# Kernel tuning notes

Measured on AMD Instinct MI355X. Metric: run time of the kernel, lower is better.

## Reference

```python
import jax, jax.numpy as jnp
import numpy as np

EMBED = 1024
HEADS = 16
HEAD_DIM = EMBED // HEADS
FFN = 4096
B, S = 2, 2048
EPS = 1e-5


def setup_inputs() -> dict:
    key = jax.random.key(0)
    ks = jax.random.split(key, 16)
    sc = 0.02
    return {
        "x": jax.random.normal(ks[0], (B, S, EMBED), jnp.float32),
        "rope_cos": jax.random.uniform(ks[1], (S, HEAD_DIM), jnp.float32),
        "rope_sin": jax.random.uniform(ks[2], (S, HEAD_DIM), jnp.float32),
        "Wq": jax.random.normal(ks[3], (EMBED, EMBED), jnp.float32) * sc,
        "bq": jnp.zeros((EMBED,), jnp.float32),
        "Wk": jax.random.normal(ks[4], (EMBED, EMBED), jnp.float32) * sc,
        "bk": jnp.zeros((EMBED,), jnp.float32),
        "Wv": jax.random.normal(ks[5], (EMBED, EMBED), jnp.float32) * sc,
        "bv": jnp.zeros((EMBED,), jnp.float32),
        "Wo": jax.random.normal(ks[6], (EMBED, EMBED), jnp.float32) * sc,
        "bo": jnp.zeros((EMBED,), jnp.float32),
        "W1": jax.random.normal(ks[7], (EMBED, FFN), jnp.float32) * sc,
        "b1": jnp.zeros((FFN,), jnp.float32),
        "W2": jax.random.normal(ks[8], (FFN, EMBED), jnp.float32) * sc,
        "b2": jnp.zeros((EMBED,), jnp.float32),
        "g1": jnp.ones((EMBED,), jnp.float32),
        "be1": jnp.zeros((EMBED,), jnp.float32),
        "g2": jnp.ones((EMBED,), jnp.float32),
        "be2": jnp.zeros((EMBED,), jnp.float32),
    }


def _layernorm(x, g, b):
    mu = jnp.mean(x, axis=-1, keepdims=True)
    var = jnp.var(x, axis=-1, keepdims=True)
    return (x - mu) * jax.lax.rsqrt(var + EPS) * g + b


def _rotate_half(x):
    half = x.shape[-1] // 2
    return jnp.concatenate((-x[..., half:], x[..., :half]), axis=-1)


def _apply_rope(x, cos, sin):
    # x: (B, H, S, D); cos/sin: (S, D)
    return x * cos[None, None] + _rotate_half(x) * sin[None, None]


def reference(x, rope_cos, rope_sin, Wq, bq, Wk, bk, Wv, bv, Wo, bo,
              W1, b1, W2, b2, g1, be1, g2, be2):
    batch, seq_len, embed = x.shape
    n = _layernorm(x, g1, be1)

    def heads(t):
        return t.reshape(batch, seq_len, HEADS, HEAD_DIM).transpose(0, 2, 1, 3)

    q = heads(n @ Wq + bq)
    k = heads(n @ Wk + bk)
    v = heads(n @ Wv + bv)
    q = _apply_rope(q, rope_cos, rope_sin)
    k = _apply_rope(k, rope_cos, rope_sin)

    scale = 1.0 / np.sqrt(HEAD_DIM)
    scores = jnp.einsum("bhqd,bhkd->bhqk", q, k) * scale  # (B,H,S,S)
    causal = jnp.triu(jnp.ones((seq_len, seq_len), bool), k=1)
    scores = jnp.where(causal[None, None], -jnp.inf, scores)
    attn = jax.nn.softmax(scores, axis=-1)
    out = jnp.einsum("bhqk,bhkd->bhqd", attn, v)
    out = out.transpose(0, 2, 1, 3).reshape(batch, seq_len, embed)
    x = x + (out @ Wo + bo)

    n2 = _layernorm(x, g2, be2)
    h = jax.nn.gelu(n2 @ W1 + b1, approximate=False)
    x = x + (h @ W2 + b2)
    return x
```

## Files before the change

kernel.cpp:

```cpp
#include <hip/hip_runtime.h>
#include <math.h>

#define EMBED 1024
#define SLEN  2048
#define BATCH 2
#define HEADS 16
#define HD    64
#define FFN_D 4096
#define MROWS (BATCH*SLEN)

typedef short bh8  __attribute__((ext_vector_type(8)));
typedef float f32x4 __attribute__((ext_vector_type(4)));
typedef __attribute__((address_space(3))) const short* lsp;

#define MFMA16(a,b,c) __builtin_amdgcn_mfma_f32_16x16x32_bf16((a),(b),(c),0,0,0)
#define GLDS16(g,l) __builtin_amdgcn_global_load_lds( \
    (__attribute__((address_space(1))) void*)(g), \
    (__attribute__((address_space(3))) void*)(l), 16, 0, 0)
#define DSR(dst, base, IMM) \
  asm volatile("ds_read_b128 %0, %1 offset:" #IMM : "=v"(dst) : "v"(base))

__device__ inline float b2f(short s) {
  union { unsigned u; float f; } c; c.u = ((unsigned)(unsigned short)s) << 16; return c.f;
}
__device__ inline short f2b(float f) {
  union { float f; unsigned u; } c; c.f = f;
  unsigned r = (c.u + 0x7FFFu + ((c.u >> 16) & 1u)) >> 16;
  return (short)r;
}
__device__ inline float exp2a(float x) {
  float r; asm("v_exp_f32 %0, %1" : "=v"(r) : "v"(x)); return r;
}

__global__ __launch_bounds__(256) void transpose_w(const float* __restrict__ in,
                                                   short* __restrict__ out,
                                                   int K, int N) {
  __shared__ short sm[64][65];
  const int tid = threadIdx.x;
  const int k0 = blockIdx.y * 64, n0 = blockIdx.x * 64;
#pragma unroll
  for (int it = 0; it < 16; ++it) {
    int idx = it * 256 + tid;
    int r = idx >> 6, c = idx & 63;
    sm[r][c] = f2b(in[(size_t)(k0 + r) * N + n0 + c]);
  }
  __syncthreads();
#pragma unroll
  for (int it = 0; it < 16; ++it) {
    int idx = it * 256 + tid;
    int r = idx >> 6, c = idx & 63;
    out[(size_t)(n0 + r) * K + k0 + c] = sm[c][r];
  }
}

__global__ __launch_bounds__(256) void transpose_v(const short* __restrict__ in,
                                                   short* __restrict__ out) {
  __shared__ short sm[64][65];
  const int tid = threadIdx.x;
  const int s0 = blockIdx.x * 64, bh = blockIdx.y;
  const int b = bh >> 4, h = bh & 15;
#pragma unroll
  for (int it = 0; it < 16; ++it) {
    int idx = it * 256 + tid;
    int r = idx >> 6, c = idx & 63;
    sm[r][c] = in[((size_t)(b*SLEN + s0 + r))*EMBED + h*HD + c];
  }
  __syncthreads();
#pragma unroll
  for (int it = 0; it < 16; ++it) {
    int idx = it * 256 + tid;
    int r = idx >> 6, c = idx & 63;
    out[((size_t)(bh*HD + r))*SLEN + s0 + c] = sm[c][r];
  }
}

__global__ __launch_bounds__(256) void ln_kernel(const float* __restrict__ inF,
                                                 const short* __restrict__ inB,
                                                 const float* __restrict__ gw,
                                                 const float* __restrict__ bw,
                                                 short* __restrict__ out) {
  const int row = blockIdx.x, tid = threadIdx.x;
  const int w = tid >> 6;
  const size_t base = (size_t)row * EMBED;
  float x[4];
#pragma unroll
  for (int i = 0; i < 4; ++i) {
    int c = tid + i * 256;
    x[i] = inF ? inF[base + c] : b2f(inB[base + c]);
  }
  float s = x[0] + x[1] + x[2] + x[3];
  float ss = x[0]*x[0] + x[1]*x[1] + x[2]*x[2] + x[3]*x[3];
#pragma unroll
  for (int off = 32; off >= 1; off >>= 1) { s += __shfl_xor(s, off); ss += __shfl_xor(ss, off); }
  __shared__ float red[8];
  if ((tid & 63) == 0) { red[w*2] = s; red[w*2+1] = ss; }
  __syncthreads();
  s  = red[0] + red[2] + red[4] + red[6];
  ss = red[1] + red[3] + red[5] + red[7];
  const float mu = s * (1.0f/EMBED);
  const float var = ss * (1.0f/EMBED) - mu*mu;
  const float rstd = rsqrtf(var + 1e-5f);
#pragma unroll
  for (int i = 0; i < 4; ++i) {
    int c = tid + i * 256;
    out[base + c] = f2b((x[i]-mu)*rstd*gw[c] + bw[c]);
  }
}

__global__ __launch_bounds__(256, 2) void gemm_bt(const short* __restrict__ A,
                                                  const short* __restrict__ Bt,
                                                  const float* __restrict__ bias0,
                                                  const float* __restrict__ bias1,
                                                  const float* __restrict__ bias2,
                                                  float* __restrict__ outF,
                                                  short* __restrict__ outB0,
                                                  short* __restrict__ outB1,
                                                  short* __restrict__ outB2,
                                                  const float* __restrict__ residF,
                                                  const short* __restrict__ residB,
                                                  const float* __restrict__ ropeCos,
                                                  const float* __restrict__ ropeSin,
                                                  int N, int K, int gelu, int qkv) {
  __shared__ short As[16384];
  __shared__ short Bs[16384];
  const int tid = threadIdx.x;
  const int w = tid >> 6, L = tid & 63;
  const int quad = L >> 4, l16 = L & 15;

  int bx = blockIdx.x, by = blockIdx.y;
  {
    const int gx = gridDim.x;
    const int nwg = gx * gridDim.y;
    const int wg = by*gx + bx;
    const int swz = (wg & 7)*(nwg >> 3) + (wg >> 3);
    bx = swz % gx; by = swz / gx;
  }
  const int bm = by * 128, bn = bx * 128;
  const int wm = (w >> 1) * 64, wn = (w & 1) * 64;
  const int NT = K >> 6;

  f32x4 acc[4][4];
#pragma unroll
  for (int i = 0; i < 4; ++i)
#pragma unroll
    for (int j = 0; j < 4; ++j) acc[i][j] = (f32x4){0.f,0.f,0.f,0.f};

  const int c0i = tid, c1i = 256 + tid;
  const int r0i = c0i >> 2, s0i = (c0i & 3) ^ ((r0i >> 1) & 3);
  const int r1i = c1i >> 2, s1i = (c1i & 3) ^ ((r1i >> 1) & 3);
  const short* aG0 = A  + (size_t)(bm + r0i)*K + s0i*8;
  const short* aG1 = A  + (size_t)(bm + r1i)*K + s1i*8;
  const short* bG0 = Bt + (size_t)(bn + r0i)*K + s0i*8;
  const short* bG1 = Bt + (size_t)(bn + r1i)*K + s1i*8;

  const int ssw = (l16 >> 1) & 3;
  lsp pA0 = (lsp)(As + (wm + l16)*32 + ((quad ^ ssw) << 3));
  lsp pB0 = (lsp)(Bs + (wn + l16)*32 + ((quad ^ ssw) << 3));
  lsp pA1 = pA0 + 8192;
  lsp pB1 = pB0 + 8192;

#define STG(DST, G0, G1, BUF, KH, KOFF) do { \
    GLDS16(G0 + (KOFF) + (KH)*32, DST + (BUF)*8192 + (KH)*4096 + w*512); \
    GLDS16(G1 + (KOFF) + (KH)*32, DST + (BUF)*8192 + (KH)*4096 + 2048 + w*512); \
  } while (0)

  STG(As, aG0, aG1, 0, 0, 0);   STG(Bs, bG0, bG1, 0, 0, 0);
  STG(As, aG0, aG1, 0, 1, 0);   STG(Bs, bG0, bG1, 0, 1, 0);
  STG(As, aG0, aG1, 1, 0, 64);  STG(Bs, bG0, bG1, 1, 0, 64);
  STG(As, aG0, aG1, 1, 1, 64);  STG(Bs, bG0, bG1, 1, 1, 64);

  for (int t = 0; t < NT; ++t) {
    const int cb = t & 1;
    lsp Ab = cb ? pA1 : pA0;
    lsp Bb = cb ? pB1 : pB0;
    const bool pf = (t + 2) < NT;
    const int kofA = (t + 2) << 6;
    bh8 af[4], bf[4];

    if (t < NT-1) asm volatile("s_waitcnt vmcnt(12)" ::: "memory");
    else          asm volatile("s_waitcnt vmcnt(4)"  ::: "memory");
    __builtin_amdgcn_s_barrier();
    DSR(af[0], Ab, 0);    DSR(af[1], Ab, 1024);
    DSR(af[2], Ab, 2048); DSR(af[3], Ab, 3072);
    DSR(bf[0], Bb, 0);    DSR(bf[1], Bb, 1024);
    DSR(bf[2], Bb, 2048); DSR(bf[3], Bb, 3072);
    asm volatile("s_waitcnt lgkmcnt(0)" ::: "memory");
    __builtin_amdgcn_sched_barrier(0);
    __builtin_amdgcn_s_barrier();
    if (pf) { STG(As, aG0, aG1, cb, 0, kofA); STG(Bs, bG0, bG1, cb, 0, kofA); }
    __builtin_amdgcn_sched_barrier(0);
    __builtin_amdgcn_s_setprio(1);
#pragma unroll
    for (int mi = 0; mi < 4; ++mi)
#pragma unroll
      for (int ni = 0; ni < 4; ++ni)
        acc[mi][ni] = MFMA16(af[mi], bf[ni], acc[mi][ni]);
    __builtin_amdgcn_s_setprio(0);

    if (t < NT-2)       asm volatile("s_waitcnt vmcnt(12)" ::: "memory");
    else if (t == NT-2) asm volatile("s_waitcnt vmcnt(8)"  ::: "memory");
    else                asm volatile("s_waitcnt vmcnt(0)"  ::: "memory");
    __builtin_amdgcn_s_barrier();
    DSR(af[0], Ab, 8192);  DSR(af[1], Ab, 9216);
    DSR(af[2], Ab, 10240); DSR(af[3], Ab, 11264);
    DSR(bf[0], Bb, 8192);  DSR(bf[1], Bb, 9216);
    DSR(bf[2], Bb, 10240); DSR(bf[3], Bb, 11264);
    asm volatile("s_waitcnt lgkmcnt(0)" ::: "memory");
    __builtin_amdgcn_sched_barrier(0);
    __builtin_amdgcn_s_barrier();
    if (pf) { STG(As, aG0, aG1, cb, 1, kofA); STG(Bs, bG0, bG1, cb, 1, kofA); }
    __builtin_amdgcn_sched_barrier(0);
    __builtin_amdgcn_s_setprio(1);
#pragma unroll
    for (int mi = 0; mi < 4; ++mi)
#pragma unroll
      for (int ni = 0; ni < 4; ++ni)
        acc[mi][ni] = MFMA16(af[mi], bf[ni], acc[mi][ni]);
    __builtin_amdgcn_s_setprio(0);
  }
#undef STG

  if (qkv) {
    const int cc = (bn + wn) >> 10;
    const float* bp = (cc == 0 ? bias0 : cc == 1 ? bias1 : bias2);
    short* ob2 = (cc == 0 ? outB0 : cc == 1 ? outB1 : outB2);
#pragma unroll
    for (int mi = 0; mi < 4; ++mi) {
      float vv[4][4];
#pragma unroll
      for (int ni = 0; ni < 4; ++ni) {
        const int colw = (bn + wn + ni*16 + l16) & 1023;
#pragma unroll
        for (int r = 0; r < 4; ++r) vv[ni][r] = acc[mi][ni][r] + bp[colw];
      }
      if (cc <= 1) {
#pragma unroll
        for (int nlo = 0; nlo < 2; ++nlo) {
          const int d = nlo*16 + l16;
#pragma unroll
          for (int r = 0; r < 4; ++r) {
            const int s = (bm + wm + mi*16 + quad*4 + r) & (SLEN - 1);
            const float c0 = ropeCos[s*HD + d],      s0 = ropeSin[s*HD + d];
            const float c1 = ropeCos[s*HD + 32 + d], s1 = ropeSin[s*HD + 32 + d];
            const float lo = vv[nlo][r], hi = vv[nlo + 2][r];
            vv[nlo][r]     = lo*c0 - hi*s0;
            vv[nlo + 2][r] = hi*c1 + lo*s1;
          }
        }
      }
#pragma unroll
      for (int ni = 0; ni < 4; ++ni) {
        const int colw = (bn + wn + ni*16 + l16) & 1023;
#pragma unroll
        for (int r = 0; r < 4; ++r) {
          const int gr = bm + wm + mi*16 + quad*4 + r;
          ob2[(size_t)gr*1024 + colw] = f2b(vv[ni][r]);
        }
      }
    }
    return;
  }
#pragma unroll
  for (int mi = 0; mi < 4; ++mi) {
#pragma unroll
    for (int ni = 0; ni < 4; ++ni) {
      const int col = bn + wn + ni*16 + l16;
      const float bv = bias0 ? bias0[col] : 0.f;
#pragma unroll
      for (int r = 0; r < 4; ++r) {
        const int gr = bm + wm + mi*16 + quad*4 + r;
        float v = acc[mi][ni][r] + bv;
        if (gelu) v = 0.5f*v*(1.f + erff(v*0.70710678f));
        if (residF) v += residF[(size_t)gr*N + col];
        if (residB) v += b2f(residB[(size_t)gr*N + col]);
        if (outF) outF[(size_t)gr*N + col] = v;
        if (outB0) outB0[(size_t)gr*N + col] = f2b(v);
      }
    }
  }
}

__global__ __launch_bounds__(256) void attn_kernel(const short* __restrict__ Qb,
                                                   const short* __restrict__ Kb,
                                                   const short* __restrict__ VT,
                                                   short* __restrict__ AOb) {
  __shared__ short Klds[2][64*72];
  __shared__ short Vlds[2][64*72];
  __shared__ short Plds[4*16*72];
  const int tid = threadIdx.x;
  const int w = tid >> 6, L = tid & 63, quad = L >> 4, l16 = L & 15;
  const int bh = blockIdx.x, qt = 31 - (int)blockIdx.y;
  const int b = bh >> 4, h = bh & 15;
  const int qbase = qt*64 + w*16;

  const size_t qrow = ((size_t)(b*SLEN + qbase + l16))*EMBED + h*HD;
  const bh8 aq0 = *(const bh8*)(Qb + qrow + quad*8);
  const bh8 aq1 = *(const bh8*)(Qb + qrow + 32 + quad*8);

  f32x4 o[4];
#pragma unroll
  for (int i = 0; i < 4; ++i) o[i] = (f32x4){0.f,0.f,0.f,0.f};
  float m_r[4] = {-1e30f,-1e30f,-1e30f,-1e30f};
  float l_r[4] = {0.f,0.f,0.f,0.f};
  const float scale2 = 0.125f * 1.44269504089f;
  const short* KgP = Kb + ((size_t)(b*SLEN))*EMBED + h*HD;
  const short* VgP = VT + ((size_t)(bh*HD))*SLEN;
  const int r0 = tid >> 3, ch = tid & 7;

  bh8 k0r, k1r, v0r, v1r;
  k0r = *(const bh8*)(KgP + (size_t)r0*EMBED + ch*8);
  k1r = *(const bh8*)(KgP + (size_t)(r0 + 32)*EMBED + ch*8);
  v0r = *(const bh8*)(VgP + (size_t)r0*SLEN + ch*8);
  v1r = *(const bh8*)(VgP + (size_t)(r0 + 32)*SLEN + ch*8);

  int cur = 0;
  for (int kt = 0; kt <= qt; ++kt) {
    short* Kl = Klds[cur];
    short* Vl = Vlds[cur];
    *(bh8*)(Kl + r0*72 + ch*8)      = k0r;
    *(bh8*)(Kl + (r0+32)*72 + ch*8) = k1r;
    *(bh8*)(Vl + r0*72 + ch*8)      = v0r;
    *(bh8*)(Vl + (r0+32)*72 + ch*8) = v1r;
    __syncthreads();
    if (kt < qt) {
      const int kk = (kt + 1)*64;
      k0r = *(const bh8*)(KgP + (size_t)(kk + r0)*EMBED + ch*8);
      k1r = *(const bh8*)(KgP + (size_t)(kk + r0 + 32)*EMBED + ch*8);
      v0r = *(const bh8*)(VgP + (size_t)r0*SLEN + kk + ch*8);
      v1r = *(const bh8*)(VgP + (size_t)(r0 + 32)*SLEN + kk + ch*8);
    }

    const int k0 = kt*64;
    f32x4 s[4];
#pragma unroll
    for (int nt = 0; nt < 4; ++nt) {
      s[nt] = (f32x4){0.f,0.f,0.f,0.f};
      const short* kp = Kl + (nt*16 + l16)*72 + quad*8;
      s[nt] = MFMA16(aq0, *(const bh8*)kp,        s[nt]);
      s[nt] = MFMA16(aq1, *(const bh8*)(kp + 32), s[nt]);
    }

    const bool lastTile = (kt == qt);
#pragma unroll
    for (int r = 0; r < 4; ++r) {
      const int q = qbase + quad*4 + r;
      float v[4];
#pragma unroll
      for (int nt = 0; nt < 4; ++nt) {
        v[nt] = s[nt][r]*scale2;
        if (lastTile && (k0 + nt*16 + l16 > q)) v[nt] = -1e30f;
      }
      float mx = fmaxf(fmaxf(v[0], v[1]), fmaxf(v[2], v[3]));
#pragma unroll
      for (int off = 8; off >= 1; off >>= 1) mx = fmaxf(mx, __shfl_xor(mx, off));
      const float mnew = fmaxf(m_r[r], mx);
      const float alpha = exp2a(m_r[r] - mnew);
      float p[4], rs = 0.f;
#pragma unroll
      for (int nt = 0; nt < 4; ++nt) { p[nt] = exp2a(v[nt] - mnew); rs += p[nt]; }
#pragma unroll
      for (int off = 8; off >= 1; off >>= 1) rs += __shfl_xor(rs, off);
      l_r[r] = l_r[r]*alpha + rs;
      m_r[r] = mnew;
#pragma unroll
      for (int dt = 0; dt < 4; ++dt) o[dt][r] *= alpha;
      short* prow = Plds + w*1152 + (quad*4 + r)*72;
#pragma unroll
      for (int nt = 0; nt < 4; ++nt) prow[nt*16 + l16] = f2b(p[nt]);
    }

    const short* pr = Plds + w*1152 + l16*72;
    const bh8 pf0 = *(const bh8*)(pr + quad*8);
    const bh8 pf1 = *(const bh8*)(pr + 32 + quad*8);
#pragma unroll
    for (int dt = 0; dt < 4; ++dt) {
      const short* vp = Vl + (dt*16 + l16)*72 + quad*8;
      o[dt] = MFMA16(pf0, *(const bh8*)vp,        o[dt]);
      o[dt] = MFMA16(pf1, *(const bh8*)(vp + 32), o[dt]);
    }
    cur ^= 1;
  }

#pragma unroll
  for (int r = 0; r < 4; ++r) {
    const float inv = 1.0f / l_r[r];
    const size_t orow = ((size_t)(b*SLEN + qbase + quad*4 + r))*EMBED + h*HD;
#pragma unroll
    for (int dt = 0; dt < 4; ++dt)
      AOb[orow + dt*16 + l16] = f2b(o[dt][r]*inv);
  }
}

extern "C" void kernel_launch(void* const* d_in, const int* in_sizes, int n_in,
                              void* d_out, int out_size, void* d_ws, size_t ws_size,
                              hipStream_t stream) {
  const float* x    = (const float*)d_in[0];
  const float* cosb = (const float*)d_in[1];
  const float* sinb = (const float*)d_in[2];
  const float* Wq = (const float*)d_in[3];  const float* bq  = (const float*)d_in[4];
  const float* Wk = (const float*)d_in[5];  const float* bk  = (const float*)d_in[6];
  const float* Wv = (const float*)d_in[7];  const float* bv  = (const float*)d_in[8];
  const float* Wo = (const float*)d_in[9];  const float* bo  = (const float*)d_in[10];
  const float* W1 = (const float*)d_in[11]; const float* b1  = (const float*)d_in[12];
  const float* W2 = (const float*)d_in[13]; const float* b2  = (const float*)d_in[14];
  const float* g1 = (const float*)d_in[15]; const float* be1 = (const float*)d_in[16];
  const float* g2 = (const float*)d_in[17]; const float* be2 = (const float*)d_in[18];
  float* out = (float*)d_out;

  char* ws = (char*)d_ws;
  const size_t MB = 1ull << 20;
  short* wqkvT = (short*)(ws + 0*MB);
  short* woT = (short*)(ws + 6*MB);
  short* w1T = (short*)(ws + 8*MB);
  short* n1b = (short*)(ws + 16*MB);
  short* Qb  = (short*)(ws + 24*MB);
  short* Kb  = (short*)(ws + 32*MB);
  short* Vb  = (short*)(ws + 40*MB);
  short* VTb = (short*)(ws + 48*MB);
  short* AOb = (short*)(ws + 56*MB);
  float* X1f = (float*)(ws + 16*MB);
  short* n2b = (short*)(ws + 0*MB);
  short* Hb  = (short*)(ws + 32*MB);
  short* w2T = (short*)(ws + 0*MB);

  transpose_w<<<dim3(16,16), 256, 0, stream>>>(Wq, wqkvT,                1024, 1024);
  transpose_w<<<dim3(16,16), 256, 0, stream>>>(Wk, wqkvT + 1024*1024,    1024, 1024);
  transpose_w<<<dim3(16,16), 256, 0, stream>>>(Wv, wqkvT + 2*1024*1024,  1024, 1024);
  transpose_w<<<dim3(16,16), 256, 0, stream>>>(Wo, woT, 1024, 1024);
  transpose_w<<<dim3(64,16), 256, 0, stream>>>(W1, w1T, 1024, 4096);

  ln_kernel<<<MROWS, 256, 0, stream>>>(x, nullptr, g1, be1, n1b);

  gemm_bt<<<dim3(24,32), 256, 0, stream>>>(n1b, wqkvT, bq, bk, bv,
                                           nullptr, Qb, Kb, Vb, nullptr, nullptr,
                                           cosb, sinb, 3072, 1024, 0, 1);

  transpose_v<<<dim3(32,32), 256, 0, stream>>>(Vb, VTb);

  attn_kernel<<<dim3(32,32), 256, 0, stream>>>(Qb, Kb, VTb, AOb);

  gemm_bt<<<dim3(8,32), 256, 0, stream>>>(AOb, woT, bo, nullptr, nullptr,
                                          X1f, nullptr, nullptr, nullptr, x, nullptr,
                                          nullptr, nullptr, 1024, 1024, 0, 0);

  ln_kernel<<<MROWS, 256, 0, stream>>>(X1f, nullptr, g2, be2, n2b);

  gemm_bt<<<dim3(32,32), 256, 0, stream>>>(n2b, w1T, b1, nullptr, nullptr,
                                           nullptr, Hb, nullptr, nullptr, nullptr, nullptr,
                                           nullptr, nullptr, 4096, 1024, 1, 0);

  transpose_w<<<dim3(16,64), 256, 0, stream>>>(W2, w2T, 4096, 1024);

  gemm_bt<<<dim3(8,32), 256, 0, stream>>>(Hb, w2T, b2, nullptr, nullptr,
                                          out, nullptr, nullptr, nullptr, X1f, nullptr,
                                          nullptr, nullptr, 1024, 4096, 0, 0);
}
```

Baseline: 425.4 us.

## Use 4-stage LDS ring with one barrier per K-slice and fast GELU

Restructures the GEMM main loop from double-buffered 64-wide K tiles with two barriers per half-step into a 4-slot ring of 32-wide K slices, prefetched three slices ahead with a single barrier per phase. The goal is to deepen load/compute overlap and cut synchronisation overhead. Separately, the erf-based GELU epilogue is replaced with a tanh-form approximation evaluated via hardware exp2 and reciprocal, trading a small accuracy loss for cheaper math.

```diff
diff --git a/kernel.cpp b/kernel.cpp
--- a/kernel.cpp
+++ b/kernel.cpp
@@ -30,6 +30,9 @@
 }
 __device__ inline float exp2a(float x) {
   float r; asm("v_exp_f32 %0, %1" : "=v"(r) : "v"(x)); return r;
+}
+__device__ inline float rcpa(float x) {
+  float r; asm("v_rcp_f32 %0, %1" : "=v"(r) : "v"(x)); return r;
 }
 
 __global__ __launch_bounds__(256) void transpose_w(const float* __restrict__ in,
@@ -137,7 +140,7 @@
   }
   const int bm = by * 128, bn = bx * 128;
   const int wm = (w >> 1) * 64, wn = (w & 1) * 64;
-  const int NT = K >> 6;
+  const int NP = K >> 5;
 
   f32x4 acc[4][4];
 #pragma unroll
@@ -156,68 +159,51 @@
   const int ssw = (l16 >> 1) & 3;
   lsp pA0 = (lsp)(As + (wm + l16)*32 + ((quad ^ ssw) << 3));
   lsp pB0 = (lsp)(Bs + (wn + l16)*32 + ((quad ^ ssw) << 3));
-  lsp pA1 = pA0 + 8192;
-  lsp pB1 = pB0 + 8192;
-
-#define STG(DST, G0, G1, BUF, KH, KOFF) do { \
-    GLDS16(G0 + (KOFF) + (KH)*32, DST + (BUF)*8192 + (KH)*4096 + w*512); \
-    GLDS16(G1 + (KOFF) + (KH)*32, DST + (BUF)*8192 + (KH)*4096 + 2048 + w*512); \
+
+#define STG(DST, G0, G1, SLOT, KOFF) do { \
+    GLDS16(G0 + (KOFF), DST + (SLOT)*4096 + w*512); \
+    GLDS16(G1 + (KOFF), DST + (SLOT)*4096 + 2048 + w*512); \
   } while (0)
 
-  STG(As, aG0, aG1, 0, 0, 0);   STG(Bs, bG0, bG1, 0, 0, 0);
-  STG(As, aG0, aG1, 0, 1, 0);   STG(Bs, bG0, bG1, 0, 1, 0);
-  STG(As, aG0, aG1, 1, 0, 64);  STG(Bs, bG0, bG1, 1, 0, 64);
-  STG(As, aG0, aG1, 1, 1, 64);  STG(Bs, bG0, bG1, 1, 1, 64);
-
-  for (int t = 0; t < NT; ++t) {
-    const int cb = t & 1;
-    lsp Ab = cb ? pA1 : pA0;
-    lsp Bb = cb ? pB1 : pB0;
-    const bool pf = (t + 2) < NT;
-    const int kofA = (t + 2) << 6;
-    bh8 af[4], bf[4];
-
-    if (t < NT-1) asm volatile("s_waitcnt vmcnt(12)" ::: "memory");
-    else          asm volatile("s_waitcnt vmcnt(4)"  ::: "memory");
-    __builtin_amdgcn_s_barrier();
-    DSR(af[0], Ab, 0);    DSR(af[1], Ab, 1024);
-    DSR(af[2], Ab, 2048); DSR(af[3], Ab, 3072);
-    DSR(bf[0], Bb, 0);    DSR(bf[1], Bb, 1024);
-    DSR(bf[2], Bb, 2048); DSR(bf[3], Bb, 3072);
-    asm volatile("s_waitcnt lgkmcnt(0)" ::: "memory");
-    __builtin_amdgcn_sched_barrier(0);
-    __builtin_amdgcn_s_barrier();
-    if (pf) { STG(As, aG0, aG1, cb, 0, kofA); STG(Bs, bG0, bG1, cb, 0, kofA); }
-    __builtin_amdgcn_sched_barrier(0);
-    __builtin_amdgcn_s_setprio(1);
-#pragma unroll
-    for (int mi = 0; mi < 4; ++mi)
-#pragma unroll
-      for (int ni = 0; ni < 4; ++ni)
-        acc[mi][ni] = MFMA16(af[mi], bf[ni], acc[mi][ni]);
-    __builtin_amdgcn_s_setprio(0);
-
-    if (t < NT-2)       asm volatile("s_waitcnt vmcnt(12)" ::: "memory");
-    else if (t == NT-2) asm volatile("s_waitcnt vmcnt(8)"  ::: "memory");
-    else                asm volatile("s_waitcnt vmcnt(0)"  ::: "memory");
-    __builtin_amdgcn_s_barrier();
-    DSR(af[0], Ab, 8192);  DSR(af[1], Ab, 9216);
-    DSR(af[2], Ab, 10240); DSR(af[3], Ab, 11264);
-    DSR(bf[0], Bb, 8192);  DSR(bf[1], Bb, 9216);
-    DSR(bf[2], Bb, 10240); DSR(bf[3], Bb, 11264);
-    asm volatile("s_waitcnt lgkmcnt(0)" ::: "memory");
-    __builtin_amdgcn_sched_barrier(0);
-    __builtin_amdgcn_s_barrier();
-    if (pf) { STG(As, aG0, aG1, cb, 1, kofA); STG(Bs, bG0, bG1, cb, 1, kofA); }
-    __builtin_amdgcn_sched_barrier(0);
-    __builtin_amdgcn_s_setprio(1);
-#pragma unroll
-    for (int mi = 0; mi < 4; ++mi)
-#pragma unroll
-      for (int ni = 0; ni < 4; ++ni)
-        acc[mi][ni] = MFMA16(af[mi], bf[ni], acc[mi][ni]);
-    __builtin_amdgcn_s_setprio(0);
-  }
+#define PH(S, AO0, AO1, AO2, AO3) do { \
+    const int p = p0 + S; \
+    const int rem = NP - 1 - p; \
+    if (rem >= 2)      asm volatile("s_waitcnt vmcnt(8)" ::: "memory"); \
+    else if (rem == 1) asm volatile("s_waitcnt vmcnt(4)" ::: "memory"); \
+    else               asm volatile("s_waitcnt vmcnt(0)" ::: "memory"); \
+    __builtin_amdgcn_s_barrier(); \
+    if (p + 3 < NP) { \
+      const int ko = (p + 3) << 5; \
+      STG(As, aG0, aG1, ((S)+3)&3, ko); \
+      STG(Bs, bG0, bG1, ((S)+3)&3, ko); \
+    } \
+    bh8 af[4], bf[4]; \
+    DSR(af[0], pA0, AO0); DSR(af[1], pA0, AO1); \
+    DSR(af[2], pA0, AO2); DSR(af[3], pA0, AO3); \
+    DSR(bf[0], pB0, AO0); DSR(bf[1], pB0, AO1); \
+    DSR(bf[2], pB0, AO2); DSR(bf[3], pB0, AO3); \
+    asm volatile("s_waitcnt lgkmcnt(0)" ::: "memory"); \
+    __builtin_amdgcn_sched_barrier(0); \
+    __builtin_amdgcn_s_setprio(1); \
+    _Pragma("unroll") \
+    for (int mi = 0; mi < 4; ++mi) \
+      _Pragma("unroll") \
+      for (int ni = 0; ni < 4; ++ni) \
+        acc[mi][ni] = MFMA16(af[mi], bf[ni], acc[mi][ni]); \
+    __builtin_amdgcn_s_setprio(0); \
+  } while (0)
+
+  STG(As, aG0, aG1, 0, 0);   STG(Bs, bG0, bG1, 0, 0);
+  STG(As, aG0, aG1, 1, 32);  STG(Bs, bG0, bG1, 1, 32);
+  STG(As, aG0, aG1, 2, 64);  STG(Bs, bG0, bG1, 2, 64);
+
+  for (int p0 = 0; p0 < NP; p0 += 4) {
+    PH(0, 0,     1024,  2048,  3072);
+    PH(1, 8192,  9216,  10240, 11264);
+    PH(2, 16384, 17408, 18432, 19456);
+    PH(3, 24576, 25600, 26624, 27648);
+  }
+#undef PH
 #undef STG
 
   if (qkv) {
@@ -270,7 +256,13 @@
       for (int r = 0; r < 4; ++r) {
         const int gr = bm + wm + mi*16 + quad*4 + r;
         float v = acc[mi][ni][r] + bv;
-        if (gelu) v = 0.5f*v*(1.f + erff(v*0.70710678f));
+        if (gelu) {
+          const float x2 = v*v;
+          float wv = v*(2.3022077f + 0.1029435f*x2);
+          wv = fminf(wv, 80.f);
+          const float tt = exp2a(wv);
+          v = v*tt*rcpa(tt + 1.f);
+        }
         if (residF) v += residF[(size_t)gr*N + col];
         if (residB) v += b2f(residB[(size_t)gr*N + col]);
         if (outF) outF[(size_t)gr*N + col] = v;
```

Measured after the change: 404.4 us. -4.9%, faster.
